# Optimization experiments

Measured on AMD Instinct MI355X. Metric: run time of the kernel, lower is better.

Reference implementation:

```python
import jax, jax.numpy as jnp
import numpy as np

B, S, D, UNITS = 64, 2048, 512, 256

def setup_inputs() -> dict:
    key = jax.random.key(0)
    ks = jax.random.split(key, 8)
    sd = 1.0 / np.sqrt(D)
    query = jax.random.normal(ks[0], (B, D), dtype=jnp.float32)
    values = jax.random.normal(ks[1], (B, S, D), dtype=jnp.float32)
    W1 = jax.random.normal(ks[2], (D, UNITS), dtype=jnp.float32) * sd
    b1 = jnp.zeros((UNITS,), dtype=jnp.float32)
    W2 = jax.random.normal(ks[3], (D, UNITS), dtype=jnp.float32) * sd
    b2 = jnp.zeros((UNITS,), dtype=jnp.float32)
    V = jax.random.normal(ks[4], (UNITS, 1), dtype=jnp.float32) * (1.0 / np.sqrt(UNITS))
    bV = jnp.zeros((1,), dtype=jnp.float32)
    return {"query": query, "values": values, "W1": W1, "b1": b1,
            "W2": W2, "b2": b2, "V": V, "bV": bV}

def reference(query, values, W1, b1, W2, b2, V, bV):
    # proj_v: [B, S, U]; proj_q: [B, 1, U]
    proj_v = jnp.einsum('bsd,du->bsu', values, W1) + b1
    proj_q = (query @ W2 + b2)[:, None, :]
    # score: [B, S, 1]
    score = jnp.tanh(proj_v + proj_q) @ V + bV
    attn = jax.nn.softmax(score, axis=1)           # softmax over sequence axis
    context = jnp.sum(attn * values, axis=1)        # [B, D]
    return context
```

## Files before the change

### kernel.cpp

```cpp
#include <hip/hip_runtime.h>

typedef unsigned short u16;
typedef unsigned int u32;
typedef __attribute__((ext_vector_type(8))) short short8;
typedef __attribute__((ext_vector_type(4))) float f32x4;

#define NB 64
#define NS 2048
#define ND 512
#define NU 256

__device__ __forceinline__ u16 f2b(float f) {
    u32 x = __float_as_uint(f);
    u32 r = (x + 0x7FFFu + ((x >> 16) & 1u)) >> 16;
    return (u16)r;
}
__device__ __forceinline__ float fast_tanh(float x) {
    float e = __expf(2.0f * x);
    return 1.0f - 2.0f / (e + 1.0f);
}

__global__ __launch_bounds__(256) void cbias_kernel(
    const float* __restrict__ q, const float* __restrict__ W2,
    const float* __restrict__ b1, const float* __restrict__ b2,
    float* __restrict__ cb)
{
    int b = blockIdx.x, u = threadIdx.x;
    __shared__ float qs[ND];
    qs[u]       = q[b * ND + u];
    qs[u + 256] = q[b * ND + u + 256];
    __syncthreads();
    float acc = 0.f;
#pragma unroll 8
    for (int d = 0; d < ND; d++)
        acc += qs[d] * W2[d * NU + u];
    cb[b * NU + u] = acc + b1[u] + b2[u];
}

__global__ __launch_bounds__(256) void transpose_kernel(
    const float* __restrict__ W1, u16* __restrict__ W1T)
{
    __shared__ float tile[64][65];
    int k0 = blockIdx.x * 64;
    int u0 = blockIdx.y * 64;
    for (int i = threadIdx.x; i < 4096; i += 256) {
        int r = i >> 6, c = i & 63;
        tile[r][c] = W1[(k0 + r) * NU + u0 + c];
    }
    __syncthreads();
    for (int i = threadIdx.x; i < 4096; i += 256) {
        int r = i >> 6, c = i & 63;
        W1T[(u0 + r) * ND + k0 + c] = f2b(tile[c][r]);
    }
}

__global__ __launch_bounds__(512) void score_kernel(
    const float* __restrict__ values,
    const u16* __restrict__ W1T,
    const float* __restrict__ cb,
    const float* __restrict__ V,
    float* __restrict__ scores)
{
    const int tid  = threadIdx.x;
    const int lane = tid & 63;
    const int wave = tid >> 6;
    const int wm   = wave >> 2;
    const int wn   = wave & 3;
    const int m16  = lane & 15;
    const int quad = lane >> 4;

    const int mblk = blockIdx.x;
    const int b    = mblk >> 4;
    const size_t base_row = (size_t)mblk * 128;

    __shared__ u16 At[128][40];
    __shared__ u16 Bt[256][40];
    __shared__ float cbs[NU];
    __shared__ float Vs[NU];
    __shared__ float rowsum[128];

    if (tid < 256) { cbs[tid] = cb[b * NU + tid]; Vs[tid] = V[tid]; }
    if (tid < 128) rowsum[tid] = 0.f;

    f32x4 acc[4][4] = {};

    const float* Abase = values + base_row * ND;
    const int arow = tid >> 2, aseg = tid & 3;

    for (int k0 = 0; k0 < ND; k0 += 32) {
        {
            const float* src = Abase + (size_t)arow * ND + k0 + aseg * 8;
            float4 v0 = *(const float4*)src;
            float4 v1 = *(const float4*)(src + 4);
            union { u16 h[8]; uint4 q; } pk;
            pk.h[0] = f2b(v0.x); pk.h[1] = f2b(v0.y);
            pk.h[2] = f2b(v0.z); pk.h[3] = f2b(v0.w);
            pk.h[4] = f2b(v1.x); pk.h[5] = f2b(v1.y);
            pk.h[6] = f2b(v1.z); pk.h[7] = f2b(v1.w);
            *(uint4*)&At[arow][aseg * 8] = pk.q;
        }
        {
            const int u = tid >> 2, seg = tid & 3;
            uint4 v0 = *(const uint4*)(W1T + (size_t)u * ND + k0 + seg * 8);
            uint4 v1 = *(const uint4*)(W1T + (size_t)(u + 128) * ND + k0 + seg * 8);
            *(uint4*)&Bt[u][seg * 8]       = v0;
            *(uint4*)&Bt[u + 128][seg * 8] = v1;
        }
        __syncthreads();

        short8 afr[4], bfr[4];
#pragma unroll
        for (int rb = 0; rb < 4; rb++)
            afr[rb] = *(const short8*)&At[wm * 64 + rb * 16 + m16][quad * 8];
#pragma unroll
        for (int cbk = 0; cbk < 4; cbk++)
            bfr[cbk] = *(const short8*)&Bt[wn * 64 + cbk * 16 + m16][quad * 8];
#pragma unroll
        for (int rb = 0; rb < 4; rb++)
#pragma unroll
            for (int cbk = 0; cbk < 4; cbk++)
                acc[rb][cbk] = __builtin_amdgcn_mfma_f32_16x16x32_bf16(
                    afr[rb], bfr[cbk], acc[rb][cbk], 0, 0, 0);
        __syncthreads();
    }

    float cbv[4], vv[4];
#pragma unroll
    for (int cbk = 0; cbk < 4; cbk++) {
        int c = wn * 64 + cbk * 16 + m16;
        cbv[cbk] = cbs[c];
        vv[cbk]  = Vs[c];
    }
#pragma unroll
    for (int rb = 0; rb < 4; rb++) {
#pragma unroll
        for (int i = 0; i < 4; i++) {
            float s = 0.f;
#pragma unroll
            for (int cbk = 0; cbk < 4; cbk++)
                s += fast_tanh(acc[rb][cbk][i] + cbv[cbk]) * vv[cbk];
            s += __shfl_xor(s, 1, 64);
            s += __shfl_xor(s, 2, 64);
            s += __shfl_xor(s, 4, 64);
            s += __shfl_xor(s, 8, 64);
            if (m16 == 0)
                atomicAdd(&rowsum[wm * 64 + rb * 16 + quad * 4 + i], s);
        }
    }
    __syncthreads();
    if (tid < 128) scores[base_row + tid] = rowsum[tid];
}

__global__ __launch_bounds__(256) void softmax_kernel(
    const float* __restrict__ scores, float* __restrict__ attn)
{
    int b = blockIdx.x, tid = threadIdx.x;
    __shared__ float red[256];
    const float* s = scores + (size_t)b * NS;
    float v[8];
    float mx = -1e30f;
#pragma unroll
    for (int i = 0; i < 8; i++) { v[i] = s[tid + i * 256]; mx = fmaxf(mx, v[i]); }
    red[tid] = mx; __syncthreads();
    for (int off = 128; off > 0; off >>= 1) {
        if (tid < off) red[tid] = fmaxf(red[tid], red[tid + off]);
        __syncthreads();
    }
    mx = red[0]; __syncthreads();
    float sum = 0.f;
#pragma unroll
    for (int i = 0; i < 8; i++) { v[i] = __expf(v[i] - mx); sum += v[i]; }
    red[tid] = sum; __syncthreads();
    for (int off = 128; off > 0; off >>= 1) {
        if (tid < off) red[tid] += red[tid + off];
        __syncthreads();
    }
    float inv = 1.0f / red[0];
#pragma unroll
    for (int i = 0; i < 8; i++) attn[(size_t)b * NS + tid + i * 256] = v[i] * inv;
}

__global__ __launch_bounds__(256) void context_kernel(
    const float* __restrict__ values, const float* __restrict__ attn,
    float* __restrict__ partial)
{
    int sc = blockIdx.x, b = blockIdx.y, tid = threadIdx.x;
    int srow = tid >> 6;
    int d0 = (tid & 63) * 8;
    __shared__ float at[128];
    __shared__ float part[4][ND];
    if (tid < 128) at[tid] = attn[(size_t)b * NS + sc * 128 + tid];
    __syncthreads();
    float acc[8] = {0.f,0.f,0.f,0.f,0.f,0.f,0.f,0.f};
    const float* vb = values + ((size_t)b * NS + (size_t)sc * 128) * ND;
#pragma unroll 4
    for (int i = 0; i < 32; i++) {
        int sl = i * 4 + srow;
        float a = at[sl];
        float4 r0 = *(const float4*)(vb + (size_t)sl * ND + d0);
        float4 r1 = *(const float4*)(vb + (size_t)sl * ND + d0 + 4);
        acc[0] += a * r0.x; acc[1] += a * r0.y;
        acc[2] += a * r0.z; acc[3] += a * r0.w;
        acc[4] += a * r1.x; acc[5] += a * r1.y;
        acc[6] += a * r1.z; acc[7] += a * r1.w;
    }
#pragma unroll
    for (int j = 0; j < 8; j++) part[srow][d0 + j] = acc[j];
    __syncthreads();
    if (tid < 128) {
#pragma unroll
        for (int j = 0; j < 4; j++) {
            int d = tid * 4 + j;
            partial[((size_t)b * 16 + sc) * ND + d] =
                part[0][d] + part[1][d] + part[2][d] + part[3][d];
        }
    }
}

__global__ __launch_bounds__(256) void finalize_kernel(
    const float* __restrict__ partial, float* __restrict__ out)
{
    int idx = blockIdx.x * 256 + threadIdx.x;
    int b = idx >> 9, d = idx & 511;
    float s = 0.f;
#pragma unroll
    for (int sc = 0; sc < 16; sc++)
        s += partial[((size_t)b * 16 + sc) * ND + d];
    out[idx] = s;
}

extern "C" void kernel_launch(void* const* d_in, const int* in_sizes, int n_in,
                              void* d_out, int out_size, void* d_ws, size_t ws_size,
                              hipStream_t stream)
{
    const float* q      = (const float*)d_in[0];
    const float* values = (const float*)d_in[1];
    const float* W1     = (const float*)d_in[2];
    const float* b1     = (const float*)d_in[3];
    const float* W2     = (const float*)d_in[4];
    const float* b2     = (const float*)d_in[5];
    const float* V      = (const float*)d_in[6];

    char* ws = (char*)d_ws;
    float* cb      = (float*)(ws);
    u16*   W1T     = (u16*)  (ws + 65536);
    float* scores  = (float*)(ws + 65536 + 262144);
    float* attn    = (float*)(ws + 851968);
    float* partial = (float*)(ws + 1376256);

    hipLaunchKernelGGL(cbias_kernel, dim3(64), dim3(256), 0, stream, q, W2, b1, b2, cb);
    hipLaunchKernelGGL(transpose_kernel, dim3(8, 4), dim3(256), 0, stream, W1, W1T);
    hipLaunchKernelGGL(score_kernel, dim3(1024), dim3(512), 0, stream,
                       values, W1T, cb, V, scores);
    hipLaunchKernelGGL(softmax_kernel, dim3(64), dim3(256), 0, stream, scores, attn);
    hipLaunchKernelGGL(context_kernel, dim3(16, 64), dim3(256), 0, stream,
                       values, attn, partial);
    hipLaunchKernelGGL(finalize_kernel, dim3(128), dim3(256), 0, stream,
                       partial, (float*)d_out);
}
```

Measured before the change: 475.2 us.

## Retile score GEMM to 64-row blocks with K=64 chunks and halve context chunks

The score kernel now uses 256-thread blocks of 64 rows with all four waves sharing the same A tile. It stages K in chunks of 64 instead of 32, which halves the number of barriers per tile. W1T is pre-laid out in contiguous per-K-chunk blocks so the B-tile load becomes straight 128-byte row copies, and fp32-to-bf16 packing uses the paired conversion intrinsic. The context kernel splits the sequence into 64-row chunks (32 per batch) with an 8-row by 4-float4 thread layout to raise parallelism, at the cost of twice as many partials for finalize to reduce and less B-tile reuse per block in the GEMM.

```diff
diff --git a/kernel.cpp b/kernel.cpp
--- a/kernel.cpp
+++ b/kernel.cpp
@@ -1,4 +1,5 @@
 #include <hip/hip_runtime.h>
+#include <hip/hip_bf16.h>
 
 typedef unsigned short u16;
 typedef unsigned int u32;
@@ -14,6 +15,10 @@
     u32 x = __float_as_uint(f);
     u32 r = (x + 0x7FFFu + ((x >> 16) & 1u)) >> 16;
     return (u16)r;
+}
+__device__ __forceinline__ u32 pk2(float lo, float hi) {
+    __hip_bfloat162 h = __float22bfloat162_rn(float2{lo, hi});
+    return *(u32*)&h;
 }
 __device__ __forceinline__ float fast_tanh(float x) {
     float e = __expf(2.0f * x);
@@ -38,7 +43,7 @@
 }
 
 __global__ __launch_bounds__(256) void transpose_kernel(
-    const float* __restrict__ W1, u16* __restrict__ W1T)
+    const float* __restrict__ W1, u16* __restrict__ W1Tc)
 {
     __shared__ float tile[64][65];
     int k0 = blockIdx.x * 64;
@@ -50,77 +55,82 @@
     __syncthreads();
     for (int i = threadIdx.x; i < 4096; i += 256) {
         int r = i >> 6, c = i & 63;
-        W1T[(u0 + r) * ND + k0 + c] = f2b(tile[c][r]);
-    }
-}
-
-__global__ __launch_bounds__(512) void score_kernel(
+        W1Tc[blockIdx.x * (NU * 64) + (u0 + r) * 64 + c] = f2b(tile[c][r]);
+    }
+}
+
+__global__ __launch_bounds__(256, 3) void score_kernel(
     const float* __restrict__ values,
-    const u16* __restrict__ W1T,
+    const u16* __restrict__ W1Tc,
     const float* __restrict__ cb,
     const float* __restrict__ V,
     float* __restrict__ scores)
 {
     const int tid  = threadIdx.x;
     const int lane = tid & 63;
-    const int wave = tid >> 6;
-    const int wm   = wave >> 2;
-    const int wn   = wave & 3;
+    const int wn   = tid >> 6;
     const int m16  = lane & 15;
     const int quad = lane >> 4;
 
     const int mblk = blockIdx.x;
-    const int b    = mblk >> 4;
-    const size_t base_row = (size_t)mblk * 128;
-
-    __shared__ u16 At[128][40];
-    __shared__ u16 Bt[256][40];
+    const int b    = mblk >> 5;
+    const size_t base_row = (size_t)mblk * 64;
+
+    __shared__ u16 At[64][72];
+    __shared__ u16 Bt[256][72];
     __shared__ float cbs[NU];
     __shared__ float Vs[NU];
-    __shared__ float rowsum[128];
-
-    if (tid < 256) { cbs[tid] = cb[b * NU + tid]; Vs[tid] = V[tid]; }
-    if (tid < 128) rowsum[tid] = 0.f;
+    __shared__ float rowsum[64];
+
+    cbs[tid] = cb[b * NU + tid];
+    Vs[tid]  = V[tid];
+    if (tid < 64) rowsum[tid] = 0.f;
 
     f32x4 acc[4][4] = {};
 
     const float* Abase = values + base_row * ND;
     const int arow = tid >> 2, aseg = tid & 3;
 
-    for (int k0 = 0; k0 < ND; k0 += 32) {
+    for (int kc = 0; kc < 8; kc++) {
+        const int k0 = kc * 64;
         {
-            const float* src = Abase + (size_t)arow * ND + k0 + aseg * 8;
-            float4 v0 = *(const float4*)src;
-            float4 v1 = *(const float4*)(src + 4);
-            union { u16 h[8]; uint4 q; } pk;
-            pk.h[0] = f2b(v0.x); pk.h[1] = f2b(v0.y);
-            pk.h[2] = f2b(v0.z); pk.h[3] = f2b(v0.w);
-            pk.h[4] = f2b(v1.x); pk.h[5] = f2b(v1.y);
-            pk.h[6] = f2b(v1.z); pk.h[7] = f2b(v1.w);
-            *(uint4*)&At[arow][aseg * 8] = pk.q;
+            const float* src = Abase + (size_t)arow * ND + k0 + aseg * 16;
+            float4 v0 = ((const float4*)src)[0];
+            float4 v1 = ((const float4*)src)[1];
+            float4 v2 = ((const float4*)src)[2];
+            float4 v3 = ((const float4*)src)[3];
+            uint4 q0, q1;
+            q0.x = pk2(v0.x, v0.y); q0.y = pk2(v0.z, v0.w);
+            q0.z = pk2(v1.x, v1.y); q0.w = pk2(v1.z, v1.w);
+            q1.x = pk2(v2.x, v2.y); q1.y = pk2(v2.z, v2.w);
+            q1.z = pk2(v3.x, v3.y); q1.w = pk2(v3.z, v3.w);
+            *(uint4*)&At[arow][aseg * 16]     = q0;
+            *(uint4*)&At[arow][aseg * 16 + 8] = q1;
         }
         {
-            const int u = tid >> 2, seg = tid & 3;
-            uint4 v0 = *(const uint4*)(W1T + (size_t)u * ND + k0 + seg * 8);
-            uint4 v1 = *(const uint4*)(W1T + (size_t)(u + 128) * ND + k0 + seg * 8);
-            *(uint4*)&Bt[u][seg * 8]       = v0;
-            *(uint4*)&Bt[u + 128][seg * 8] = v1;
-        }
-        __syncthreads();
-
-        short8 afr[4], bfr[4];
-#pragma unroll
-        for (int rb = 0; rb < 4; rb++)
-            afr[rb] = *(const short8*)&At[wm * 64 + rb * 16 + m16][quad * 8];
-#pragma unroll
-        for (int cbk = 0; cbk < 4; cbk++)
-            bfr[cbk] = *(const short8*)&Bt[wn * 64 + cbk * 16 + m16][quad * 8];
-#pragma unroll
-        for (int rb = 0; rb < 4; rb++)
+            const uint4* bsrc = (const uint4*)(W1Tc + (size_t)kc * (NU * 64) + tid * 64);
+#pragma unroll
+            for (int j = 0; j < 8; j++)
+                *(uint4*)&Bt[tid][j * 8] = bsrc[j];
+        }
+        __syncthreads();
+
+#pragma unroll
+        for (int kh = 0; kh < 2; kh++) {
+            short8 afr[4], bfr[4];
+#pragma unroll
+            for (int rb = 0; rb < 4; rb++)
+                afr[rb] = *(const short8*)&At[rb * 16 + m16][kh * 32 + quad * 8];
 #pragma unroll
             for (int cbk = 0; cbk < 4; cbk++)
-                acc[rb][cbk] = __builtin_amdgcn_mfma_f32_16x16x32_bf16(
-                    afr[rb], bfr[cbk], acc[rb][cbk], 0, 0, 0);
+                bfr[cbk] = *(const short8*)&Bt[wn * 64 + cbk * 16 + m16][kh * 32 + quad * 8];
+#pragma unroll
+            for (int rb = 0; rb < 4; rb++)
+#pragma unroll
+                for (int cbk = 0; cbk < 4; cbk++)
+                    acc[rb][cbk] = __builtin_amdgcn_mfma_f32_16x16x32_bf16(
+                        afr[rb], bfr[cbk], acc[rb][cbk], 0, 0, 0);
+        }
         __syncthreads();
     }
 
@@ -144,11 +154,11 @@
             s += __shfl_xor(s, 4, 64);
             s += __shfl_xor(s, 8, 64);
             if (m16 == 0)
-                atomicAdd(&rowsum[wm * 64 + rb * 16 + quad * 4 + i], s);
-        }
-    }
-    __syncthreads();
-    if (tid < 128) scores[base_row + tid] = rowsum[tid];
+                atomicAdd(&rowsum[rb * 16 + quad * 4 + i], s);
+        }
+    }
+    __syncthreads();
+    if (tid < 64) scores[base_row + tid] = rowsum[tid];
 }
 
 __global__ __launch_bounds__(256) void softmax_kernel(
@@ -185,35 +195,38 @@
     float* __restrict__ partial)
 {
     int sc = blockIdx.x, b = blockIdx.y, tid = threadIdx.x;
-    int srow = tid >> 6;
-    int d0 = (tid & 63) * 8;
-    __shared__ float at[128];
-    __shared__ float part[4][ND];
-    if (tid < 128) at[tid] = attn[(size_t)b * NS + sc * 128 + tid];
-    __syncthreads();
-    float acc[8] = {0.f,0.f,0.f,0.f,0.f,0.f,0.f,0.f};
-    const float* vb = values + ((size_t)b * NS + (size_t)sc * 128) * ND;
-#pragma unroll 4
-    for (int i = 0; i < 32; i++) {
-        int sl = i * 4 + srow;
+    int srow = tid >> 5;
+    int dcol = tid & 31;
+    __shared__ float at[64];
+    __shared__ float part[8][ND];
+    if (tid < 64) at[tid] = attn[(size_t)b * NS + sc * 64 + tid];
+    __syncthreads();
+    float acc[16] = {};
+    const float* vb = values + ((size_t)b * NS + (size_t)sc * 64) * ND;
+#pragma unroll 2
+    for (int i = 0; i < 8; i++) {
+        int sl = i * 8 + srow;
         float a = at[sl];
-        float4 r0 = *(const float4*)(vb + (size_t)sl * ND + d0);
-        float4 r1 = *(const float4*)(vb + (size_t)sl * ND + d0 + 4);
-        acc[0] += a * r0.x; acc[1] += a * r0.y;
-        acc[2] += a * r0.z; acc[3] += a * r0.w;
-        acc[4] += a * r1.x; acc[5] += a * r1.y;
-        acc[6] += a * r1.z; acc[7] += a * r1.w;
-    }
-#pragma unroll
-    for (int j = 0; j < 8; j++) part[srow][d0 + j] = acc[j];
-    __syncthreads();
-    if (tid < 128) {
-#pragma unroll
-        for (int j = 0; j < 4; j++) {
-            int d = tid * 4 + j;
-            partial[((size_t)b * 16 + sc) * ND + d] =
-                part[0][d] + part[1][d] + part[2][d] + part[3][d];
-        }
+        const float* row = vb + (size_t)sl * ND + dcol * 4;
+        float4 r0 = *(const float4*)(row);
+        float4 r1 = *(const float4*)(row + 128);
+        float4 r2 = *(const float4*)(row + 256);
+        float4 r3 = *(const float4*)(row + 384);
+        acc[0]  += a * r0.x; acc[1]  += a * r0.y; acc[2]  += a * r0.z; acc[3]  += a * r0.w;
+        acc[4]  += a * r1.x; acc[5]  += a * r1.y; acc[6]  += a * r1.z; acc[7]  += a * r1.w;
+        acc[8]  += a * r2.x; acc[9]  += a * r2.y; acc[10] += a * r2.z; acc[11] += a * r2.w;
+        acc[12] += a * r3.x; acc[13] += a * r3.y; acc[14] += a * r3.z; acc[15] += a * r3.w;
+    }
+#pragma unroll
+    for (int j = 0; j < 4; j++)
+        *(float4*)&part[srow][j * 128 + dcol * 4] =
+            float4{acc[j*4], acc[j*4+1], acc[j*4+2], acc[j*4+3]};
+    __syncthreads();
+    for (int d = tid; d < ND; d += 256) {
+        float s = 0.f;
+#pragma unroll
+        for (int r = 0; r < 8; r++) s += part[r][d];
+        partial[((size_t)b * 32 + sc) * ND + d] = s;
     }
 }
 
@@ -224,8 +237,8 @@
     int b = idx >> 9, d = idx & 511;
     float s = 0.f;
 #pragma unroll
-    for (int sc = 0; sc < 16; sc++)
-        s += partial[((size_t)b * 16 + sc) * ND + d];
+    for (int sc = 0; sc < 32; sc++)
+        s += partial[((size_t)b * 32 + sc) * ND + d];
     out[idx] = s;
 }
 
@@ -243,17 +256,17 @@
 
     char* ws = (char*)d_ws;
     float* cb      = (float*)(ws);
-    u16*   W1T     = (u16*)  (ws + 65536);
-    float* scores  = (float*)(ws + 65536 + 262144);
+    u16*   W1Tc    = (u16*)  (ws + 65536);
+    float* scores  = (float*)(ws + 327680);
     float* attn    = (float*)(ws + 851968);
     float* partial = (float*)(ws + 1376256);
 
     hipLaunchKernelGGL(cbias_kernel, dim3(64), dim3(256), 0, stream, q, W2, b1, b2, cb);
-    hipLaunchKernelGGL(transpose_kernel, dim3(8, 4), dim3(256), 0, stream, W1, W1T);
-    hipLaunchKernelGGL(score_kernel, dim3(1024), dim3(512), 0, stream,
-                       values, W1T, cb, V, scores);
+    hipLaunchKernelGGL(transpose_kernel, dim3(8, 4), dim3(256), 0, stream, W1, W1Tc);
+    hipLaunchKernelGGL(score_kernel, dim3(2048), dim3(256), 0, stream,
+                       values, W1Tc, cb, V, scores);
     hipLaunchKernelGGL(softmax_kernel, dim3(64), dim3(256), 0, stream, scores, attn);
-    hipLaunchKernelGGL(context_kernel, dim3(16, 64), dim3(256), 0, stream,
+    hipLaunchKernelGGL(context_kernel, dim3(32, 64), dim3(256), 0, stream,
                        values, attn, partial);
     hipLaunchKernelGGL(finalize_kernel, dim3(128), dim3(256), 0, stream,
                        partial, (float*)d_out);
```

Result: slower. 485.7 us (+2.2%).
